# Kernel optimization log

Measured on AMD Instinct MI355X. Metric: run time of the kernel, lower is better.

Reference implementation:

```python
import jax, jax.numpy as jnp
import numpy as np

N_NODES = 100000
N_EDGES = 800000
IN_DIM = 128
OUT_DIM = 128


def setup_inputs() -> dict:
    key = jax.random.key(0)
    k_h, k_w, k_src, k_dst = jax.random.split(key, 4)
    h = jax.random.normal(k_h, (N_NODES, IN_DIM), dtype=jnp.float32)
    # xavier_normal_ with relu gain ~ sqrt(2) * sqrt(2/(fan_in+fan_out))
    gain = np.sqrt(2.0)
    std = gain * np.sqrt(2.0 / (IN_DIM + OUT_DIM))
    W = jax.random.normal(k_w, (OUT_DIM, IN_DIM), dtype=jnp.float32) * std
    src = jax.random.randint(k_src, (N_EDGES,), 0, N_NODES, dtype=jnp.int64)
    dst = jax.random.randint(k_dst, (N_EDGES,), 0, N_NODES, dtype=jnp.int64)
    return {"h": h, "W": W, "src": src, "dst": dst}


def reference(h, W, src, dst):
    # fc + ReLU is applied per-edge to the gathered src feature, then summed
    # over incoming edges per dst node. Since fc acts on src features only,
    # project once per node ([N, in] @ [in, out]) then gather per edge.
    proj = jax.nn.relu(jnp.matmul(h, W.T))          # [N, out_dim]
    msgs = proj[src]                                 # [E, out_dim] (gather)
    out = jax.ops.segment_sum(msgs, dst, num_segments=N_NODES)  # [N, out_dim]
    return out
```

## Files before the change

### kernel.cpp

```cpp
#include <hip/hip_runtime.h>
#include <hip/hip_bf16.h>

#define IN_DIM 128
#define OUT_DIM 128
#define CAP 32

typedef __attribute__((ext_vector_type(8))) short short8;
typedef __attribute__((ext_vector_type(8))) unsigned short ushort8;
typedef __attribute__((ext_vector_type(4))) float floatx4;

__device__ __forceinline__ unsigned short f2bf(float x) {
    union { float f; unsigned int u; } a; a.f = x;
    unsigned int u = a.u;
    unsigned int r = (u + 0x7fffu + ((u >> 16) & 1u)) >> 16;
    return (unsigned short)r;
}
__device__ __forceinline__ ushort2 f2bf2(float x, float y) {
    __hip_bfloat162 h2 = __float22bfloat162_rn(make_float2(x, y));
    union { __hip_bfloat162 h; ushort2 u; } c; c.h = h2; return c.u;
}
__device__ __forceinline__ float bf_lo(unsigned int v) {
    union { unsigned int u; float f; } a; a.u = v << 16; return a.f;
}
__device__ __forceinline__ float bf_hi(unsigned int v) {
    union { unsigned int u; float f; } a; a.u = v & 0xffff0000u; return a.f;
}

#define APAD 136

__global__ __launch_bounds__(256) void fused_proj_bucket(
    const float* __restrict__ h, const float* __restrict__ W,
    unsigned short* __restrict__ projb,
    const int* __restrict__ src, const int* __restrict__ dst,
    int* __restrict__ counts, int* __restrict__ edges,
    int M, int E)
{
    __shared__ unsigned short As[64][APAD];
    __shared__ unsigned short Bs[128][APAD];

    const int t    = threadIdx.x;
    const int wave = t >> 6;
    const int lane = t & 63;
    const int block_m = blockIdx.x * 64;
    const int gtid = blockIdx.x * 256 + t;
    const int T    = gridDim.x * 256;

    int e0 = gtid, e1 = gtid + T;
    int d0 = 0, d1 = 0, s0 = 0, s1 = 0, p0 = CAP, p1 = CAP;
    const bool v0 = e0 < E, v1 = e1 < E;
    if (v0) { d0 = dst[e0]; s0 = src[e0]; }
    if (v1) { d1 = dst[e1]; s1 = src[e1]; }
    if (v0) p0 = atomicAdd(&counts[d0], 1);
    if (v1) p1 = atomicAdd(&counts[d1], 1);

#pragma unroll
    for (int p = 0; p < 8; p++) {
        int c = p * 256 + t;
        int row = c >> 5;
        int ch  = c & 31;
        int gm = block_m + row;
        float4 v = make_float4(0.f, 0.f, 0.f, 0.f);
        if (gm < M) v = *(const float4*)&h[(size_t)gm * IN_DIM + ch * 4];
        ushort2 lo = f2bf2(v.x, v.y), hi = f2bf2(v.z, v.w);
        ushort4 b; b.x = lo.x; b.y = lo.y; b.z = hi.x; b.w = hi.y;
        *(ushort4*)&As[row][ch * 4] = b;
    }
#pragma unroll
    for (int p = 0; p < 16; p++) {
        int c = p * 256 + t;
        int row = c >> 5;
        int ch  = c & 31;
        float4 v = *(const float4*)&W[(size_t)row * IN_DIM + ch * 4];
        ushort2 lo = f2bf2(v.x, v.y), hi = f2bf2(v.z, v.w);
        ushort4 b; b.x = lo.x; b.y = lo.y; b.z = hi.x; b.w = hi.y;
        *(ushort4*)&Bs[row][ch * 4] = b;
    }

    if (v0 && p0 < CAP) edges[d0 * CAP + p0] = s0;
    if (v1 && p1 < CAP) edges[d1 * CAP + p1] = s1;
    for (int e = gtid + 2 * T; e < E; e += T) {
        int d = dst[e];
        int pos = atomicAdd(&counts[d], 1);
        if (pos < CAP) edges[d * CAP + pos] = src[e];
    }

    __syncthreads();

    const int mrow = wave * 16 + (lane & 15);
    const int kq   = (lane >> 4) * 8;
    floatx4 acc[8] = {};

#pragma unroll
    for (int ks = 0; ks < 4; ks++) {
        short8 a = *(const short8*)&As[mrow][ks * 32 + kq];
#pragma unroll
        for (int nt = 0; nt < 8; nt++) {
            short8 b = *(const short8*)&Bs[nt * 16 + (lane & 15)][ks * 32 + kq];
            acc[nt] = __builtin_amdgcn_mfma_f32_16x16x32_bf16(a, b, acc[nt], 0, 0, 0);
        }
    }

    __syncthreads();
    {
        const int rloc = wave * 16 + (lane >> 4) * 4;
        const int col  = lane & 15;
#pragma unroll
        for (int nt = 0; nt < 8; nt++)
#pragma unroll
            for (int i = 0; i < 4; i++)
                As[rloc + i][nt * 16 + col] = f2bf(fmaxf(acc[nt][i], 0.f));
    }
    __syncthreads();
#pragma unroll
    for (int q = 0; q < 4; q++) {
        int c = q * 256 + t;
        int row = c >> 4;
        int ch  = c & 15;
        int gm = block_m + row;
        if (gm < M) {
            ushort8 v = *(const ushort8*)&As[row][ch * 8];
            *(ushort8*)&projb[(size_t)gm * OUT_DIM + ch * 8] = v;
        }
    }
}

__global__ __launch_bounds__(256) void gather_kernel(const unsigned short* __restrict__ projb,
                                                     const int* __restrict__ edges,
                                                     const int* __restrict__ counts,
                                                     float* __restrict__ out, int M) {
    const int node = blockIdx.x * 4 + (threadIdx.x >> 6);
    const int lane = threadIdx.x & 63;
    if (node >= M) return;

    int cnt = counts[node];
    if (cnt > CAP) cnt = CAP;
    const int beg = node * CAP;
    const unsigned int* base = (const unsigned int*)projb;

    float a0 = 0.f, a1 = 0.f;
    int i = 0;
    for (; i + 4 <= cnt; i += 4) {
        int s0 = edges[beg + i + 0];
        int s1 = edges[beg + i + 1];
        int s2 = edges[beg + i + 2];
        int s3 = edges[beg + i + 3];
        unsigned int w0 = base[(size_t)s0 * 64 + lane];
        unsigned int w1 = base[(size_t)s1 * 64 + lane];
        unsigned int w2 = base[(size_t)s2 * 64 + lane];
        unsigned int w3 = base[(size_t)s3 * 64 + lane];
        a0 += bf_lo(w0); a1 += bf_hi(w0);
        a0 += bf_lo(w1); a1 += bf_hi(w1);
        a0 += bf_lo(w2); a1 += bf_hi(w2);
        a0 += bf_lo(w3); a1 += bf_hi(w3);
    }
    for (; i < cnt; i++) {
        int s = edges[beg + i];
        unsigned int w = base[(size_t)s * 64 + lane];
        a0 += bf_lo(w); a1 += bf_hi(w);
    }

    *(float2*)&out[(size_t)node * OUT_DIM + lane * 2] = make_float2(a0, a1);
}

extern "C" void kernel_launch(void* const* d_in, const int* in_sizes, int n_in,
                              void* d_out, int out_size, void* d_ws, size_t ws_size,
                              hipStream_t stream) {
    const float* h   = (const float*)d_in[0];
    const float* W   = (const float*)d_in[1];
    const int*   src = (const int*)d_in[2];
    const int*   dst = (const int*)d_in[3];
    float* out = (float*)d_out;

    const int M = in_sizes[0] / IN_DIM;
    const int E = in_sizes[2];

    char* ws = (char*)d_ws;
    unsigned short* projb = (unsigned short*)ws;
    size_t off = (size_t)M * OUT_DIM * sizeof(unsigned short);
    off = (off + 255) & ~(size_t)255;
    int* counts = (int*)(ws + off);  off += (size_t)M * sizeof(int);
    off = (off + 255) & ~(size_t)255;
    int* edges  = (int*)(ws + off);  off += (size_t)M * CAP * sizeof(int);

    hipMemsetAsync(counts, 0, (size_t)M * sizeof(int), stream);

    fused_proj_bucket<<<(M + 63) / 64, 256, 0, stream>>>(h, W, projb, src, dst,
                                                         counts, edges, M, E);

    gather_kernel<<<(M + 3) / 4, 256, 0, stream>>>(projb, edges, counts, out, M);
}
```

Measured before the change: 204.0 us.

## Pre-pack W into MFMA fragment bf16 layout, drop Bs LDS tile, fold memset

A new prep kernel zeroes the counts array and converts W once into bf16 laid out in MFMA B-fragment order, replacing the separate memset. The fused kernel then reads B fragments straight from global memory (L2/L1-resident) instead of every block converting W into a large shared tile. This cuts LDS use, allowing more resident blocks (launch bounds set to 5). The edge bucketing is moved after the projection store. The cost is an extra kernel launch and repeated global loads of Wb inside the MFMA loop.

```diff
diff --git a/kernel.cpp b/kernel.cpp
--- a/kernel.cpp
+++ b/kernel.cpp
@@ -28,15 +28,43 @@
 
 #define APAD 136
 
-__global__ __launch_bounds__(256) void fused_proj_bucket(
-    const float* __restrict__ h, const float* __restrict__ W,
+__global__ __launch_bounds__(256) void prep_kernel(const float* __restrict__ W,
+                                                   unsigned short* __restrict__ Wb,
+                                                   int* __restrict__ counts,
+                                                   int M, int nz) {
+    if ((int)blockIdx.x < nz) {
+        int i = blockIdx.x * 256 + threadIdx.x;
+        if (i < M) counts[i] = 0;
+    } else {
+#pragma unroll
+        for (int q = 0; q < 8; q++) {
+            int g = q * 256 + threadIdx.x;
+            int fragid = g >> 6;
+            int lane   = g & 63;
+            int nt = fragid >> 2, ks = fragid & 3;
+            int row = nt * 16 + (lane & 15);
+            int col = ks * 32 + (lane >> 4) * 8;
+            const float* s = &W[(size_t)row * IN_DIM + col];
+            float4 v0 = *(const float4*)s;
+            float4 v1 = *(const float4*)(s + 4);
+            ushort2 ab = f2bf2(v0.x, v0.y), cd = f2bf2(v0.z, v0.w);
+            ushort2 ef = f2bf2(v1.x, v1.y), gh = f2bf2(v1.z, v1.w);
+            ushort8 o;
+            o[0] = ab.x; o[1] = ab.y; o[2] = cd.x; o[3] = cd.y;
+            o[4] = ef.x; o[5] = ef.y; o[6] = gh.x; o[7] = gh.y;
+            *(ushort8*)&Wb[(size_t)g * 8] = o;
+        }
+    }
+}
+
+__global__ __launch_bounds__(256, 5) void fused_proj_bucket(
+    const float* __restrict__ h, const unsigned short* __restrict__ Wb,
     unsigned short* __restrict__ projb,
     const int* __restrict__ src, const int* __restrict__ dst,
     int* __restrict__ counts, int* __restrict__ edges,
     int M, int E)
 {
     __shared__ unsigned short As[64][APAD];
-    __shared__ unsigned short Bs[128][APAD];
 
     const int t    = threadIdx.x;
     const int wave = t >> 6;
@@ -65,24 +93,6 @@
         ushort4 b; b.x = lo.x; b.y = lo.y; b.z = hi.x; b.w = hi.y;
         *(ushort4*)&As[row][ch * 4] = b;
     }
-#pragma unroll
-    for (int p = 0; p < 16; p++) {
-        int c = p * 256 + t;
-        int row = c >> 5;
-        int ch  = c & 31;
-        float4 v = *(const float4*)&W[(size_t)row * IN_DIM + ch * 4];
-        ushort2 lo = f2bf2(v.x, v.y), hi = f2bf2(v.z, v.w);
-        ushort4 b; b.x = lo.x; b.y = lo.y; b.z = hi.x; b.w = hi.y;
-        *(ushort4*)&Bs[row][ch * 4] = b;
-    }
-
-    if (v0 && p0 < CAP) edges[d0 * CAP + p0] = s0;
-    if (v1 && p1 < CAP) edges[d1 * CAP + p1] = s1;
-    for (int e = gtid + 2 * T; e < E; e += T) {
-        int d = dst[e];
-        int pos = atomicAdd(&counts[d], 1);
-        if (pos < CAP) edges[d * CAP + pos] = src[e];
-    }
 
     __syncthreads();
 
@@ -95,7 +105,7 @@
         short8 a = *(const short8*)&As[mrow][ks * 32 + kq];
 #pragma unroll
         for (int nt = 0; nt < 8; nt++) {
-            short8 b = *(const short8*)&Bs[nt * 16 + (lane & 15)][ks * 32 + kq];
+            short8 b = *(const short8*)&Wb[(size_t)((nt * 4 + ks) * 64 + lane) * 8];
             acc[nt] = __builtin_amdgcn_mfma_f32_16x16x32_bf16(a, b, acc[nt], 0, 0, 0);
         }
     }
@@ -121,6 +131,14 @@
             ushort8 v = *(const ushort8*)&As[row][ch * 8];
             *(ushort8*)&projb[(size_t)gm * OUT_DIM + ch * 8] = v;
         }
+    }
+
+    if (v0 && p0 < CAP) edges[d0 * CAP + p0] = s0;
+    if (v1 && p1 < CAP) edges[d1 * CAP + p1] = s1;
+    for (int e = gtid + 2 * T; e < E; e += T) {
+        int d = dst[e];
+        int pos = atomicAdd(&counts[d], 1);
+        if (pos < CAP) edges[d * CAP + pos] = src[e];
     }
 }
 
@@ -181,10 +199,14 @@
     int* counts = (int*)(ws + off);  off += (size_t)M * sizeof(int);
     off = (off + 255) & ~(size_t)255;
     int* edges  = (int*)(ws + off);  off += (size_t)M * CAP * sizeof(int);
-
-    hipMemsetAsync(counts, 0, (size_t)M * sizeof(int), stream);
-
-    fused_proj_bucket<<<(M + 63) / 64, 256, 0, stream>>>(h, W, projb, src, dst,
+    off = (off + 255) & ~(size_t)255;
+    unsigned short* Wb = (unsigned short*)(ws + off);  off += 32 * 1024;
+
+    const int nz = (M + 255) / 256;
+
+    prep_kernel<<<nz + 1, 256, 0, stream>>>(W, Wb, counts, M, nz);
+
+    fused_proj_bucket<<<(M + 63) / 64, 256, 0, stream>>>(h, Wb, projb, src, dst,
                                                          counts, edges, M, E);
 
     gather_kernel<<<(M + 3) / 4, 256, 0, stream>>>(projb, edges, counts, out, M);
```

After: 205.6 us. No clear change (+0.8%).
